# Performance work log

Measured on AMD Instinct MI355X. Metric: run time of the kernel, lower is better.

## Reference

```python
import math
import jax, jax.numpy as jnp
import numpy as np

D_EMBD = 1024
N_HEAD = 16
BLOCK = 2048
B, T = 4, 2048


def setup_inputs() -> dict:
    key = jax.random.key(0)
    ks = jax.random.split(key, 5)
    d = D_EMBD
    return {
        "x": jax.random.normal(ks[0], (B, T, d), dtype=jnp.float32),
        "Wq": jax.random.normal(ks[1], (d, d), dtype=jnp.float32),
        "bq": jnp.zeros((d,), dtype=jnp.float32),
        "Wk": jax.random.normal(ks[2], (d, d), dtype=jnp.float32),
        "bk": jnp.zeros((d,), dtype=jnp.float32),
        "Wv": jax.random.normal(ks[3], (d, d), dtype=jnp.float32),
        "bv": jnp.zeros((d,), dtype=jnp.float32),
        "Wp": jax.random.normal(ks[4], (d, d), dtype=jnp.float32),
        "bp": jnp.zeros((d,), dtype=jnp.float32),
    }


def reference(x, Wq, bq, Wk, bk, Wv, bv, Wp, bp):
    Bb, Tt, C = x.shape
    n_head = N_HEAD
    hd = C // n_head  # head dim
    # QKV projections -> [B, H, T, hd]
    def split_heads(y):
        return y.reshape(Bb, Tt, n_head, hd).transpose(0, 2, 1, 3)
    Q = split_heads(x @ Wq + bq)
    K = split_heads(x @ Wk + bk)
    V = split_heads(x @ Wv + bv)
    # scores [B, H, T, T]
    attn = jnp.einsum('bhqd,bhkd->bhqk', Q, K) / math.sqrt(hd)
    # causal mask: -inf strictly above diagonal (matches triu(ones*-inf, 1))
    causal = jnp.tril(jnp.ones((Tt, Tt), dtype=bool))
    attn = jnp.where(causal, attn, -jnp.inf)
    attn = jax.nn.softmax(attn, axis=-1)
    y = jnp.einsum('bhqk,bhkd->bhqd', attn, V)
    y = y.transpose(0, 2, 1, 3).reshape(Bb, Tt, C)
    return y @ Wp + bp
```

## Files before the change

kernel.cpp:

```cpp
#include <hip/hip_runtime.h>
#include <stdint.h>
#include <stddef.h>

#define TT 2048
#define CC 1024
#define BBATCH 4
#define HH 16
#define HD 64
#define MTOT (BBATCH * TT)

typedef __bf16 bf16_t;
typedef __bf16 bf16x4 __attribute__((ext_vector_type(4)));
typedef __bf16 bf16x8 __attribute__((ext_vector_type(8)));
typedef float f32x4 __attribute__((ext_vector_type(4)));
typedef float f32x16 __attribute__((ext_vector_type(16)));

typedef const __attribute__((address_space(1))) uint32_t* as1_u32p;
typedef __attribute__((address_space(3))) uint32_t* as3_u32p;

__device__ __forceinline__ f32x4 mfma16(bf16x8 a, bf16x8 b, f32x4 c) {
  return __builtin_amdgcn_mfma_f32_16x16x32_bf16(a, b, c, 0, 0, 0);
}
__device__ __forceinline__ f32x16 mfma32(bf16x8 a, bf16x8 b, f32x16 c) {
  return __builtin_amdgcn_mfma_f32_32x32x16_bf16(a, b, c, 0, 0, 0);
}

__device__ __forceinline__ float fast_exp2(float x) {
#if __has_builtin(__builtin_amdgcn_exp2f)
  return __builtin_amdgcn_exp2f(x);
#else
  return __expf(x * 0.69314718f);
#endif
}

__device__ __forceinline__ void gload_lds16(void* lds, const void* g) {
  __builtin_amdgcn_global_load_lds((as1_u32p)g, (as3_u32p)lds, 16, 0, 0);
}

__device__ __forceinline__ bf16x8 rd32(const char* t, int row, int lane) {
  int sl = (lane >> 4) ^ ((row >> 1) & 3);
  return *(const bf16x8*)(t + row * 64 + sl * 16);
}
__device__ __forceinline__ bf16x8 rd32r(const char* t, int row, int slot) {
  return *(const bf16x8*)(t + row * 128 + ((slot ^ (row & 7)) * 16));
}

__global__ void split_x_kernel(const float* __restrict__ x, bf16_t* __restrict__ xh,
                               bf16_t* __restrict__ xl, int n4) {
  int stride = gridDim.x * blockDim.x;
  for (int i = blockIdx.x * blockDim.x + threadIdx.x; i < n4; i += stride) {
    float4 v = ((const float4*)x)[i];
    float vv[4] = {v.x, v.y, v.z, v.w};
    bf16x4 hv, lv;
#pragma unroll
    for (int j = 0; j < 4; ++j) {
      bf16_t h = (bf16_t)vv[j];
      hv[j] = h;
      lv[j] = (bf16_t)(vv[j] - (float)h);
    }
    *(bf16x4*)(xh + (size_t)i * 4) = hv;
    *(bf16x4*)(xl + (size_t)i * 4) = lv;
  }
}

__global__ void transpose_split_kernel(const float* __restrict__ Wq, const float* __restrict__ Wk,
                                       const float* __restrict__ Wv, const float* __restrict__ Wp,
                                       bf16_t* __restrict__ wqkh, bf16_t* __restrict__ wqkl,
                                       bf16_t* __restrict__ wv_t, bf16_t* __restrict__ wp_t) {
  __shared__ float tile[32][33];
  int mat = blockIdx.z;
  const float* W = (mat == 0) ? Wq : (mat == 1) ? Wk : (mat == 2) ? Wv : Wp;
  int tx = threadIdx.x, ty = threadIdx.y;
  int n0 = blockIdx.x * 32, k0 = blockIdx.y * 32;
#pragma unroll
  for (int j = 0; j < 32; j += 8)
    tile[ty + j][tx] = W[(size_t)(k0 + ty + j) * CC + n0 + tx];
  __syncthreads();
#pragma unroll
  for (int j = 0; j < 32; j += 8) {
    float v = tile[tx][ty + j];
    int n = n0 + ty + j, k = k0 + tx;
    if (mat <= 1) {
      bf16_t h = (bf16_t)v;
      size_t o = (size_t)(mat * CC + n) * CC + k;
      wqkh[o] = h;
      wqkl[o] = (bf16_t)(v - (float)h);
    } else {
      bf16_t* dst = (mat == 2) ? wv_t : wp_t;
      dst[(size_t)n * CC + k] = (bf16_t)v;
    }
  }
}

__global__ __launch_bounds__(512, 2) void gemm_qk_kernel(
    const bf16_t* __restrict__ Ah, const bf16_t* __restrict__ Al,
    const bf16_t* __restrict__ Bh, const bf16_t* __restrict__ Bl,
    const float* __restrict__ bq, const float* __restrict__ bk,
    bf16_t* __restrict__ qh, bf16_t* __restrict__ ql,
    bf16_t* __restrict__ kh, bf16_t* __restrict__ kl) {
  __shared__ __align__(16) char s_ah[2][16384];
  __shared__ __align__(16) char s_al[2][16384];
  __shared__ __align__(16) char s_bh[2][16384];
  __shared__ __align__(16) char s_bl[2][16384];

  const int blk = blockIdx.x;
  const int bn = blk & 7;
  const int bm = blk >> 3;
  const int tid = threadIdx.x, w = tid >> 6, lane = tid & 63;
  const int wr = w >> 2, wc = w & 3;
  const int qi = lane & 15, hi = lane >> 4;

  const int c0 = w * 2, c1 = w * 2 + 1;
  const int srow0 = c0 * 16 + (lane >> 2);
  const int srow1 = c1 * 16 + (lane >> 2);
  const int ssl0 = (lane & 3) ^ ((srow0 >> 1) & 3);
  const int ssl1 = (lane & 3) ^ ((srow1 >> 1) & 3);
  const size_t a_off0 = (size_t)(bm * 256 + srow0) * CC + ssl0 * 8;
  const size_t a_off1 = (size_t)(bm * 256 + srow1) * CC + ssl1 * 8;
  const size_t b_off0 = (size_t)(bn * 256 + srow0) * CC + ssl0 * 8;
  const size_t b_off1 = (size_t)(bn * 256 + srow1) * CC + ssl1 * 8;

  f32x4 acc[8][4] = {};

#define STAGE_QK(buf, k0)                                        \
  do {                                                           \
    gload_lds16(s_ah[buf] + c0 * 1024, Ah + a_off0 + (k0));      \
    gload_lds16(s_ah[buf] + c1 * 1024, Ah + a_off1 + (k0));      \
    gload_lds16(s_al[buf] + c0 * 1024, Al + a_off0 + (k0));      \
    gload_lds16(s_al[buf] + c1 * 1024, Al + a_off1 + (k0));      \
    gload_lds16(s_bh[buf] + c0 * 1024, Bh + b_off0 + (k0));      \
    gload_lds16(s_bh[buf] + c1 * 1024, Bh + b_off1 + (k0));      \
    gload_lds16(s_bl[buf] + c0 * 1024, Bl + b_off0 + (k0));      \
    gload_lds16(s_bl[buf] + c1 * 1024, Bl + b_off1 + (k0));      \
  } while (0)

  STAGE_QK(0, 0);
  int cur = 0;
  for (int ks = 0; ks < 32; ++ks) {
    if (ks < 31) {
      STAGE_QK(cur ^ 1, (ks + 1) * 32);
      asm volatile("s_waitcnt vmcnt(8)" ::: "memory");
    } else {
      asm volatile("s_waitcnt vmcnt(0)" ::: "memory");
    }
    __builtin_amdgcn_s_barrier();

    bf16x8 bfh[4], bfl[4];
#pragma unroll
    for (int ni = 0; ni < 4; ++ni) {
      int br = wc * 64 + ni * 16 + qi;
      bfh[ni] = rd32(s_bh[cur], br, lane);
      bfl[ni] = rd32(s_bl[cur], br, lane);
    }
    __builtin_amdgcn_s_setprio(1);
#pragma unroll
    for (int mi = 0; mi < 8; ++mi) {
      int ar = wr * 128 + mi * 16 + qi;
      bf16x8 ahf = rd32(s_ah[cur], ar, lane);
      bf16x8 alf = rd32(s_al[cur], ar, lane);
#pragma unroll
      for (int ni = 0; ni < 4; ++ni) {
        acc[mi][ni] = mfma16(ahf, bfh[ni], acc[mi][ni]);
        acc[mi][ni] = mfma16(ahf, bfl[ni], acc[mi][ni]);
        acc[mi][ni] = mfma16(alf, bfh[ni], acc[mi][ni]);
      }
    }
    __builtin_amdgcn_s_setprio(0);
    asm volatile("s_waitcnt lgkmcnt(0)" ::: "memory");
    __builtin_amdgcn_s_barrier();
    cur ^= 1;
  }
#undef STAGE_QK

  const int which = bn >> 2;
  const float* bias = which ? bk : bq;
  bf16_t* oh = which ? kh : qh;
  bf16_t* ol = which ? kl : ql;
#pragma unroll
  for (int mi = 0; mi < 8; ++mi) {
#pragma unroll
    for (int ni = 0; ni < 4; ++ni) {
      const int col = bn * 256 + wc * 64 + ni * 16 + qi;
      const int c1i = col & 1023;
      const int h = c1i >> 6, d = c1i & 63;
#pragma unroll
      for (int r = 0; r < 4; ++r) {
        const int row = bm * 256 + wr * 128 + mi * 16 + hi * 4 + r;
        const int b = row >> 11, t = row & 2047;
        float v = acc[mi][ni][r] + bias[c1i];
        if (!which) v *= 0.18033688f;
        const size_t off = ((size_t)(b * HH + h) * TT + t) * HD + d;
        bf16_t hv = (bf16_t)v;
        oh[off] = hv;
        ol[off] = (bf16_t)(v - (float)hv);
      }
    }
  }
}

template <int MODE>
__global__ __launch_bounds__(256) void gemm_kernel(
    const bf16_t* __restrict__ Ah,
    const bf16_t* __restrict__ Bh,
    const float* __restrict__ bias0,
    void* __restrict__ out0) {
  __shared__ __align__(16) char smem[2 * 8192];
  char* sAh = smem;
  char* sBh = smem + 8192;

  const int bn = blockIdx.x, bm = blockIdx.y;
  const int tid = threadIdx.x, w = tid >> 6, lane = tid & 63;
  const int wr = w >> 1, wc = w & 1;

  f32x4 acc[4][4] = {};

  for (int ks = 0; ks < 32; ++ks) {
    const int k0 = ks * 32;
    __syncthreads();
#pragma unroll
    for (int it = 0; it < 2; ++it) {
      int c = it * 4 + w;
      int row = c * 16 + (lane >> 2);
      int sl = (lane & 3) ^ ((row >> 1) & 3);
      size_t aoff = (size_t)(bm * 128 + row) * CC + k0 + sl * 8;
      size_t boff = (size_t)(bn * 128 + row) * CC + k0 + sl * 8;
      gload_lds16(sAh + c * 1024, Ah + aoff);
      gload_lds16(sBh + c * 1024, Bh + boff);
    }
    __syncthreads();

    bf16x8 afh[4], bfh[4];
#pragma unroll
    for (int i = 0; i < 4; ++i) {
      int ar = wr * 64 + i * 16 + (lane & 15);
      int br = wc * 64 + i * 16 + (lane & 15);
      afh[i] = rd32(sAh, ar, lane);
      bfh[i] = rd32(sBh, br, lane);
    }
#pragma unroll
    for (int mi = 0; mi < 4; ++mi) {
#pragma unroll
      for (int ni = 0; ni < 4; ++ni) {
        acc[mi][ni] = mfma16(afh[mi], bfh[ni], acc[mi][ni]);
      }
    }
  }

#pragma unroll
  for (int mi = 0; mi < 4; ++mi) {
#pragma unroll
    for (int ni = 0; ni < 4; ++ni) {
      const int col = bn * 128 + wc * 64 + ni * 16 + (lane & 15);
#pragma unroll
      for (int r = 0; r < 4; ++r) {
        const int row = bm * 128 + wr * 64 + mi * 16 + (lane >> 4) * 4 + r;
        float v = acc[mi][ni][r];
        if (MODE == 1) {
          const int h = col >> 6, d = col & 63;
          const int b = row >> 11, t = row & 2047;
          float vv = v + bias0[col];
          ((bf16_t*)out0)[((size_t)(b * HH + h) * HD + d) * TT + t] = (bf16_t)vv;
        } else {
          ((float*)out0)[(size_t)row * CC + col] = v + bias0[col];
        }
      }
    }
  }
}

__global__ __launch_bounds__(256, 3) void attn_kernel(
    const bf16_t* __restrict__ qh, const bf16_t* __restrict__ ql,
    const bf16_t* __restrict__ kh, const bf16_t* __restrict__ kl,
    const bf16_t* __restrict__ vt, bf16_t* __restrict__ y) {
  __shared__ __align__(16) char s_kh[2][8192];
  __shared__ __align__(16) char s_kl[2][8192];
  __shared__ __align__(16) char s_vt[2][8192];

  const int blk = blockIdx.x;
  const int qb = 15 - (blk >> 6);
  const int bh = (blk & 7) * 8 + ((blk >> 3) & 7);
  const int b = bh >> 4, h = bh & 15;
  const int tid = threadIdx.x, w = tid >> 6, lane = tid & 63;
  const int l31 = lane & 31, hi = lane >> 5;

  const int strow0 = w * 16 + (lane >> 3);
  const int strow1 = strow0 + 8;
  const int sl0 = (lane & 7) ^ (strow0 & 7);
  const int sl1 = (lane & 7) ^ (strow1 & 7);
  const int ksrow0 = (strow0 & ~12) | ((strow0 & 4) << 1) | ((strow0 & 8) >> 1);
  const int ksrow1 = (strow1 & ~12) | ((strow1 & 4) << 1) | ((strow1 & 8) >> 1);
  const size_t koff0 = ((size_t)bh * TT + ksrow0) * HD + sl0 * 8;
  const size_t koff1 = ((size_t)bh * TT + ksrow1) * HD + sl1 * 8;
  const size_t voff0 = ((size_t)bh * HD + strow0) * TT + sl0 * 8;
  const size_t voff1 = ((size_t)bh * HD + strow1) * TT + sl1 * 8;
  const int ch0 = (w * 2) * 1024, ch1 = (w * 2 + 1) * 1024;

#define STAGE_ATTN(buf, kt)                                                  \
  do {                                                                       \
    gload_lds16(s_kh[buf] + ch0, kh + koff0 + (size_t)(kt) * 64 * HD);       \
    gload_lds16(s_kh[buf] + ch1, kh + koff1 + (size_t)(kt) * 64 * HD);       \
    gload_lds16(s_kl[buf] + ch0, kl + koff0 + (size_t)(kt) * 64 * HD);       \
    gload_lds16(s_kl[buf] + ch1, kl + koff1 + (size_t)(kt) * 64 * HD);       \
    gload_lds16(s_vt[buf] + ch0, vt + voff0 + (size_t)(kt) * 64);            \
    gload_lds16(s_vt[buf] + ch1, vt + voff1 + (size_t)(kt) * 64);            \
  } while (0)

  const int ktmax = 2 * qb + 1;
  const int qrow0 = qb * 128 + w * 32;
  const int qv = qrow0 + l31;

  bf16x8 qhf[4], qlf[4];
#pragma unroll
  for (int kc = 0; kc < 4; ++kc) {
    size_t off = ((size_t)bh * TT + qv) * HD + kc * 16 + hi * 8;
    qhf[kc] = *(const bf16x8*)(qh + off);
    qlf[kc] = *(const bf16x8*)(ql + off);
  }

  f32x16 o0 = {}, o1 = {};
  float m = -1e30f, l = 0.f;

  STAGE_ATTN(0, 0);
  int cur = 0;
  for (int kt = 0; kt <= ktmax; ++kt) {
    if (kt < ktmax) {
      STAGE_ATTN(cur ^ 1, kt + 1);
      asm volatile("s_waitcnt vmcnt(6)" ::: "memory");
    } else {
      asm volatile("s_waitcnt vmcnt(0)" ::: "memory");
    }
    __builtin_amdgcn_s_barrier();

    const char* ckh = s_kh[cur];
    const char* ckl = s_kl[cur];
    const char* cvt = s_vt[cur];
    const bool active = (qrow0 + 31 >= kt * 64);
    if (active) {
      f32x16 s0 = {}, s1 = {};
#pragma unroll
      for (int kc = 0; kc < 4; ++kc) {
        bf16x8 kfh = rd32r(ckh, l31, kc * 2 + hi);
        bf16x8 kfl = rd32r(ckl, l31, kc * 2 + hi);
        s0 = mfma32(kfh, qhf[kc], s0);
        s0 = mfma32(kfl, qhf[kc], s0);
        s0 = mfma32(kfh, qlf[kc], s0);
      }
#pragma unroll
      for (int kc = 0; kc < 4; ++kc) {
        bf16x8 kfh = rd32r(ckh, 32 + l31, kc * 2 + hi);
        bf16x8 kfl = rd32r(ckl, 32 + l31, kc * 2 + hi);
        s1 = mfma32(kfh, qhf[kc], s1);
        s1 = mfma32(kfl, qhf[kc], s1);
        s1 = mfma32(kfh, qlf[kc], s1);
      }

      if (kt * 64 + 63 > qrow0) {
#pragma unroll
        for (int r = 0; r < 16; ++r) {
          const int kvb = kt * 64 + (r & 7) + 8 * hi + 16 * (r >> 3);
          if (kvb > qv) s0[r] = -1e30f;
          if (kvb + 32 > qv) s1[r] = -1e30f;
        }
      }

      float t8[8];
#pragma unroll
      for (int r = 0; r < 8; ++r)
        t8[r] = fmaxf(fmaxf(s0[r], s0[r + 8]), fmaxf(s1[r], s1[r + 8]));
      float t4a = fmaxf(t8[0], t8[4]), t4b = fmaxf(t8[1], t8[5]);
      float t4c = fmaxf(t8[2], t8[6]), t4d = fmaxf(t8[3], t8[7]);
      float tmax = fmaxf(fmaxf(t4a, t4b), fmaxf(t4c, t4d));
      tmax = fmaxf(tmax, __shfl_xor(tmax, 32));

      const float mnew = fmaxf(m, tmax);
      if (!__all(tmax <= m)) {
        const float sc = fast_exp2(m - mnew);
        l *= sc;
#pragma unroll
        for (int r = 0; r < 16; ++r) { o0[r] *= sc; o1[r] *= sc; }
        m = mnew;
      }

#pragma unroll
      for (int r = 0; r < 16; ++r) {
        s0[r] = fast_exp2(s0[r] - m);
        s1[r] = fast_exp2(s1[r] - m);
      }
      float p8[8];
#pragma unroll
      for (int r = 0; r < 8; ++r)
        p8[r] = (s0[r] + s0[r + 8]) + (s1[r] + s1[r + 8]);
      float ps = ((p8[0] + p8[1]) + (p8[2] + p8[3])) + ((p8[4] + p8[5]) + (p8[6] + p8[7]));
      ps += __shfl_xor(ps, 32);
      l += ps;

      bf16x8 pa[4];
#pragma unroll
      for (int cc = 0; cc < 4; ++cc) {
#pragma unroll
        for (int j = 0; j < 8; ++j)
          pa[cc][j] = (bf16_t)((cc >> 1) ? s1[8 * (cc & 1) + j] : s0[8 * (cc & 1) + j]);
      }

#pragma unroll
      for (int cc = 0; cc < 4; ++cc) {
        bf16x8 vf0 = rd32r(cvt, l31, cc * 2 + hi);
        bf16x8 vf1 = rd32r(cvt, 32 + l31, cc * 2 + hi);
        o0 = mfma32(vf0, pa[cc], o0);
        o1 = mfma32(vf1, pa[cc], o1);
      }
    }

    asm volatile("s_waitcnt lgkmcnt(0)" ::: "memory");
    __builtin_amdgcn_s_barrier();
    cur ^= 1;
  }

  const float inv = 1.f / l;
  bf16_t* yb = y + (size_t)(b * TT + qv) * CC + h * HD;
#pragma unroll
  for (int g = 0; g < 4; ++g) {
    bf16x4 ov0, ov1;
#pragma unroll
    for (int r = 0; r < 4; ++r) {
      ov0[r] = (bf16_t)(o0[g * 4 + r] * inv);
      ov1[r] = (bf16_t)(o1[g * 4 + r] * inv);
    }
    *(bf16x4*)(yb + g * 8 + hi * 4) = ov0;
    *(bf16x4*)(yb + 32 + g * 8 + hi * 4) = ov1;
  }
#undef STAGE_ATTN
}

extern "C" void kernel_launch(void* const* d_in, const int* in_sizes, int n_in,
                              void* d_out, int out_size, void* d_ws, size_t ws_size,
                              hipStream_t stream) {
  (void)in_sizes; (void)n_in; (void)out_size; (void)ws_size;
  const float* x  = (const float*)d_in[0];
  const float* Wq = (const float*)d_in[1];
  const float* bq = (const float*)d_in[2];
  const float* Wk = (const float*)d_in[3];
  const float* bk = (const float*)d_in[4];
  const float* Wv = (const float*)d_in[5];
  const float* bv = (const float*)d_in[6];
  const float* Wp = (const float*)d_in[7];
  const float* bp = (const float*)d_in[8];

  char* ws = (char*)d_ws;
  const size_t MB = 1024 * 1024;
  bf16_t* xh   = (bf16_t*)(ws + 0 * MB);
  bf16_t* xl   = (bf16_t*)(ws + 16 * MB);
  bf16_t* wqkh = (bf16_t*)(ws + 32 * MB);
  bf16_t* wqkl = (bf16_t*)(ws + 36 * MB);
  bf16_t* wv_t = (bf16_t*)(ws + 40 * MB);
  bf16_t* wp_t = (bf16_t*)(ws + 42 * MB);
  bf16_t* qhw  = (bf16_t*)(ws + 44 * MB);
  bf16_t* qlw  = (bf16_t*)(ws + 60 * MB);
  bf16_t* khw  = (bf16_t*)(ws + 76 * MB);
  bf16_t* klw  = (bf16_t*)(ws + 92 * MB);
  bf16_t* vtw  = (bf16_t*)(ws + 108 * MB);
  bf16_t* yw   = (bf16_t*)(ws + 124 * MB);

  split_x_kernel<<<2048, 256, 0, stream>>>(x, xh, xl, MTOT * CC / 4);
  transpose_split_kernel<<<dim3(32, 32, 4), dim3(32, 8), 0, stream>>>(
      Wq, Wk, Wv, Wp, wqkh, wqkl, wv_t, wp_t);
  gemm_qk_kernel<<<256, 512, 0, stream>>>(
      xh, xl, wqkh, wqkl, bq, bk, qhw, qlw, khw, klw);
  gemm_kernel<1><<<dim3(8, 64), 256, 0, stream>>>(
      xh, wv_t, bv, vtw);
  attn_kernel<<<1024, 256, 0, stream>>>(qhw, qlw, khw, klw, vtw, yw);
  gemm_kernel<2><<<dim3(8, 64), 256, 0, stream>>>(
      yw, wp_t, bp, d_out);
}
```

Measured before the change: 244.3 us.

## Double-buffer LDS tiles in projection GEMM to overlap global loads with MFMA

The projection GEMM kernel now uses two LDS buffers for the A and B tiles. It issues the next K-slice's global-to-LDS loads before computing on the current slice, and waits with explicit vmcnt counters and raw barriers instead of syncthreads. This is meant to hide global memory latency behind the MFMA work. In exchange it doubles LDS use, which may lower occupancy, and it depends on hand-written waitcnt counts being correct.

```diff
diff --git a/kernel.cpp b/kernel.cpp
--- a/kernel.cpp
+++ b/kernel.cpp
@@ -204,38 +204,51 @@
     const bf16_t* __restrict__ Bh,
     const float* __restrict__ bias0,
     void* __restrict__ out0) {
-  __shared__ __align__(16) char smem[2 * 8192];
-  char* sAh = smem;
-  char* sBh = smem + 8192;
+  __shared__ __align__(16) char s_a[2][8192];
+  __shared__ __align__(16) char s_b[2][8192];
 
   const int bn = blockIdx.x, bm = blockIdx.y;
   const int tid = threadIdx.x, w = tid >> 6, lane = tid & 63;
   const int wr = w >> 1, wc = w & 1;
 
+  const int c0 = w, c1 = w + 4;
+  const int srow0 = c0 * 16 + (lane >> 2);
+  const int srow1 = c1 * 16 + (lane >> 2);
+  const int ssl0 = (lane & 3) ^ ((srow0 >> 1) & 3);
+  const int ssl1 = (lane & 3) ^ ((srow1 >> 1) & 3);
+  const size_t a_off0 = (size_t)(bm * 128 + srow0) * CC + ssl0 * 8;
+  const size_t a_off1 = (size_t)(bm * 128 + srow1) * CC + ssl1 * 8;
+  const size_t b_off0 = (size_t)(bn * 128 + srow0) * CC + ssl0 * 8;
+  const size_t b_off1 = (size_t)(bn * 128 + srow1) * CC + ssl1 * 8;
+
   f32x4 acc[4][4] = {};
 
+#define STAGE_G2(buf, k0)                                       \
+  do {                                                          \
+    gload_lds16(s_a[buf] + c0 * 1024, Ah + a_off0 + (k0));      \
+    gload_lds16(s_a[buf] + c1 * 1024, Ah + a_off1 + (k0));      \
+    gload_lds16(s_b[buf] + c0 * 1024, Bh + b_off0 + (k0));      \
+    gload_lds16(s_b[buf] + c1 * 1024, Bh + b_off1 + (k0));      \
+  } while (0)
+
+  STAGE_G2(0, 0);
+  int cur = 0;
   for (int ks = 0; ks < 32; ++ks) {
-    const int k0 = ks * 32;
-    __syncthreads();
-#pragma unroll
-    for (int it = 0; it < 2; ++it) {
-      int c = it * 4 + w;
-      int row = c * 16 + (lane >> 2);
-      int sl = (lane & 3) ^ ((row >> 1) & 3);
-      size_t aoff = (size_t)(bm * 128 + row) * CC + k0 + sl * 8;
-      size_t boff = (size_t)(bn * 128 + row) * CC + k0 + sl * 8;
-      gload_lds16(sAh + c * 1024, Ah + aoff);
-      gload_lds16(sBh + c * 1024, Bh + boff);
-    }
-    __syncthreads();
+    if (ks < 31) {
+      STAGE_G2(cur ^ 1, (ks + 1) * 32);
+      asm volatile("s_waitcnt vmcnt(4)" ::: "memory");
+    } else {
+      asm volatile("s_waitcnt vmcnt(0)" ::: "memory");
+    }
+    __builtin_amdgcn_s_barrier();
 
     bf16x8 afh[4], bfh[4];
 #pragma unroll
     for (int i = 0; i < 4; ++i) {
       int ar = wr * 64 + i * 16 + (lane & 15);
       int br = wc * 64 + i * 16 + (lane & 15);
-      afh[i] = rd32(sAh, ar, lane);
-      bfh[i] = rd32(sBh, br, lane);
+      afh[i] = rd32(s_a[cur], ar, lane);
+      bfh[i] = rd32(s_b[cur], br, lane);
     }
 #pragma unroll
     for (int mi = 0; mi < 4; ++mi) {
@@ -244,7 +257,11 @@
         acc[mi][ni] = mfma16(afh[mi], bfh[ni], acc[mi][ni]);
       }
     }
-  }
+    asm volatile("s_waitcnt lgkmcnt(0)" ::: "memory");
+    __builtin_amdgcn_s_barrier();
+    cur ^= 1;
+  }
+#undef STAGE_G2
 
 #pragma unroll
   for (int mi = 0; mi < 4; ++mi) {
```

Measured after the change: 253.9 us. 3.9% more time.
